# Performance work log

Hardware: AMD Instinct MI355X
Metric: run time of the kernel (lower is better)

Reference implementation:

```python
import jax, jax.numpy as jnp
import numpy as np

ALPHA = 0.3          # triplet margin
LOSS_WEIGHT = 1.0
VALID_COST = 100.0   # chosen so all queries are valid (query2gt ~ U[0,1))
POS_T = 3            # pos_thresh
NEG_T = 30           # neg_thresh
EPS = 1e-6           # torch pairwise_distance eps


def setup_inputs() -> dict:
    key0 = jax.random.key(0)
    ks = jax.random.split(key0, 6)
    Nq, V, K, D, G = 2048, 6, 4096, 256, 64
    attn = jax.random.normal(ks[0], (Nq, V, K), dtype=jnp.float32)
    query2gt = jax.random.uniform(ks[1], (Nq, G), dtype=jnp.float32)  # min < VALID_COST always
    query = jax.random.normal(ks[2], (Nq, V, D), dtype=jnp.float32)
    key = jax.random.normal(ks[3], (K, V, D), dtype=jnp.float32)
    pos_idx = jax.random.randint(ks[4], (V * Nq,), 0, POS_T, dtype=jnp.int64 if jax.config.jax_enable_x64 else jnp.int32)
    neg_idx = jax.random.randint(ks[5], (V * Nq,), POS_T, NEG_T, dtype=jnp.int64 if jax.config.jax_enable_x64 else jnp.int32)
    return {"attn": attn, "query2gt": query2gt, "query": query, "key": key,
            "pos_idx": pos_idx, "neg_idx": neg_idx}


def reference(attn, query2gt, query, key, pos_idx, neg_idx):
    # valid filtering: query2gt.min(-1) < VALID_COST is all-True by construction,
    # so no rows are dropped (keeps shapes static under jit).
    q = jnp.transpose(query, (1, 0, 2))   # [V, Nq, D]
    k = jnp.transpose(key, (1, 0, 2))     # [V, K, D]
    a = jnp.transpose(attn, (1, 0, 2))    # [V, Nq, K]
    V, Nq, K = a.shape

    # batched euclidean cdist per view via gram expansion
    qq = jnp.sum(q * q, axis=-1)[:, :, None]          # [V, Nq, 1]
    kk = jnp.sum(k * k, axis=-1)[:, None, :]          # [V, 1, K]
    d2 = qq + kk - 2.0 * jnp.einsum('vnd,vkd->vnk', q, k)
    dist = jnp.sqrt(jnp.maximum(d2, 0.0))             # [V, Nq, K]

    sorted_idx = jnp.argsort(dist, axis=-1).reshape(V * Nq, K)
    a = a.reshape(V * Nq, K)
    r = jnp.arange(V * Nq)

    pos = jax.nn.sigmoid(a[r, sorted_idx[r, pos_idx]])  # [V*Nq]
    neg = jax.nn.sigmoid(a[r, sorted_idx[r, neg_idx]])  # [V*Nq]

    # TripletMarginLoss(margin=ALPHA, p=1) with anchor = ones, 1-d embeddings
    d_pos = jnp.abs(1.0 - pos + EPS)
    d_neg = jnp.abs(1.0 - neg + EPS)
    loss = jnp.mean(jnp.maximum(d_pos - d_neg + ALPHA, 0.0))
    return LOSS_WEIGHT * loss
```

## Files before the change

### kernel.cpp

```cpp
#include <hip/hip_runtime.h>
#include <stdint.h>

#define NQ    2048
#define VV    6
#define KCNT  4096
#define DD    256
#define NROWS (VV*NQ)
#define ALPHA_M 0.3f
#define EPSL  1e-6f
#define SBIAS 256.0f
#define ZTHR  2.05f
#define CAP   256
#define LCAP  16

#define TM 128
#define TN 128
#define BKK 32

typedef _Float16 f16x8 __attribute__((ext_vector_type(8)));
typedef _Float16 f16x4 __attribute__((ext_vector_type(4)));
typedef float    f32x4 __attribute__((ext_vector_type(4)));

__device__ __forceinline__ void gload16(const void* g, void* l) {
    __builtin_amdgcn_global_load_lds(
        (__attribute__((address_space(1))) void*)(uintptr_t)g,
        (__attribute__((address_space(3))) void*)(uintptr_t)(uint32_t)(uintptr_t)l,
        16, 0, 0);
}

__device__ __forceinline__ unsigned ord16(_Float16 h) {
    unsigned short b = __builtin_bit_cast(unsigned short, h);
    return (b & 0x8000u) ? (unsigned)(~b & 0xFFFFu) : (unsigned)(b | 0x8000u);
}

__device__ __forceinline__ float triplet_term(const float* attn, int r, int kpos, int kneg) {
    int v = r / NQ, q = r - v * NQ;
    float apos = attn[(size_t)q * (VV*KCNT) + v*KCNT + kpos];
    float aneg = attn[(size_t)q * (VV*KCNT) + v*KCNT + kneg];
    float pv = 1.0f / (1.0f + expf(-apos));
    float nv = 1.0f / (1.0f + expf(-aneg));
    float dp = fabsf(1.0f - pv + EPSL);
    float dn = fabsf(1.0f - nv + EPSL);
    return fmaxf(dp - dn + ALPHA_M, 0.0f);
}

__global__ __launch_bounds__(256) void pack_k_kernel(const float* __restrict__ key,
                                                     _Float16* __restrict__ Bpack,
                                                     float* __restrict__ kkp)
{
    int wid  = threadIdx.x >> 6;
    int lane = threadIdx.x & 63;
    int rowid = blockIdx.x * 4 + wid;
    int k = rowid / 6;
    int v = rowid - k * 6;
    float4 x = *(const float4*)(key + (size_t)rowid * DD + lane * 4);
    f16x4 h;
    h.x = (_Float16)x.x; h.y = (_Float16)x.y;
    h.z = (_Float16)x.z; h.w = (_Float16)x.w;
    *(f16x4*)(Bpack + ((size_t)(v * KCNT + k)) * DD + lane * 4) = h;

    float s = x.x*x.x + x.y*x.y + x.z*x.z + x.w*x.w;
    #pragma unroll
    for (int off = 32; off >= 1; off >>= 1) s += __shfl_xor(s, off);
    if (lane == 0) kkp[v * KCNT + k] = s;
}

__global__ __launch_bounds__(256) void pack_q_kernel(const float* __restrict__ query,
                                                     _Float16* __restrict__ Apack,
                                                     float* __restrict__ Trow)
{
    int wid  = threadIdx.x >> 6;
    int lane = threadIdx.x & 63;
    int rowid = blockIdx.x * 4 + wid;
    int q = rowid / 6;
    int v = rowid - q * 6;
    float4 x = *(const float4*)(query + (size_t)rowid * DD + lane * 4);
    f16x4 h;
    h.x = (_Float16)x.x; h.y = (_Float16)x.y;
    h.z = (_Float16)x.z; h.w = (_Float16)x.w;
    *(f16x4*)(Apack + ((size_t)(v * NQ + q)) * DD + lane * 4) = h;

    float qq = x.x*x.x + x.y*x.y + x.z*x.z + x.w*x.w;
    #pragma unroll
    for (int off = 32; off >= 1; off >>= 1) qq += __shfl_xor(qq, off);
    if (lane == 0) {
        float sd = sqrtf(512.0f + 4.0f * qq);
        Trow[v * NQ + q] = 256.0f - ZTHR * sd;
    }
}

__global__ __launch_bounds__(256) void score_gemm(const _Float16* __restrict__ Apack,
                                                  const _Float16* __restrict__ Bpack,
                                                  const float* __restrict__ kkp,
                                                  const float* __restrict__ Trow,
                                                  unsigned* __restrict__ cnt,
                                                  unsigned* __restrict__ cand)
{
    __shared__ _Float16 As[TM * BKK];
    __shared__ _Float16 Bs[TN * BKK];
    __shared__ unsigned lcnt[TM];

    int tid  = threadIdx.x;
    int wid  = tid >> 6;
    int lane = tid & 63;
    int c0   = blockIdx.x * TN;
    int grow = blockIdx.y * TM;
    int v    = grow / NQ;
    int q0   = grow - v * NQ;

    int srow = (wid << 4) + (lane >> 2);
    int sseg = (lane & 3) ^ ((lane >> 2) & 3);
    const _Float16* Ag0 = Apack + ((size_t)(v*NQ   + q0 + srow)) * DD + sseg*8;
    const _Float16* Ag1 = Ag0 + (size_t)64 * DD;
    const _Float16* Bg0 = Bpack + ((size_t)(v*KCNT + c0 + srow)) * DD + sseg*8;
    const _Float16* Bg1 = Bg0 + (size_t)64 * DD;

    _Float16* lA0 = As + wid*512;
    _Float16* lA1 = As + 2048 + wid*512;
    _Float16* lB0 = Bs + wid*512;
    _Float16* lB1 = Bs + 2048 + wid*512;

    int fr = lane & 15;
    int kg = lane >> 4;
    int rb = (wid >> 1) * 64;
    int cb = (wid & 1) * 64;
    int ksw = (kg ^ (fr & 3)) << 3;

    f32x4 acc[4][4] = {};

    for (int kb = 0; kb < DD; kb += BKK) {
        __syncthreads();
        gload16(Ag0 + kb, lA0);
        gload16(Ag1 + kb, lA1);
        gload16(Bg0 + kb, lB0);
        gload16(Bg1 + kb, lB1);
        __syncthreads();

        f16x8 af[4], bf[4];
        #pragma unroll
        for (int m = 0; m < 4; ++m)
            af[m] = *(const f16x8*)&As[(rb + m*16 + fr)*BKK + ksw];
        #pragma unroll
        for (int n = 0; n < 4; ++n)
            bf[n] = *(const f16x8*)&Bs[(cb + n*16 + fr)*BKK + ksw];
        #pragma unroll
        for (int m = 0; m < 4; ++m)
            #pragma unroll
            for (int n = 0; n < 4; ++n)
                acc[m][n] = __builtin_amdgcn_mfma_f32_16x16x32_f16(af[m], bf[n], acc[m][n], 0, 0, 0);
    }

    int rg = lane >> 4;
    float kkv[4];
    #pragma unroll
    for (int n = 0; n < 4; ++n)
        kkv[n] = kkp[v*KCNT + c0 + cb + n*16 + fr];

    __syncthreads();
    unsigned* lbuf = (unsigned*)As;
    if (tid < TM) lcnt[tid] = 0;
    __syncthreads();

    #pragma unroll
    for (int m = 0; m < 4; ++m) {
        #pragma unroll
        for (int j = 0; j < 4; ++j) {
            int lr = rb + m*16 + rg*4 + j;
            float Tr = Trow[grow + lr];
            #pragma unroll
            for (int n = 0; n < 4; ++n) {
                float s = kkv[n] - 2.0f * acc[m][n][j];
                if (s < Tr) {
                    unsigned pos = atomicAdd(&lcnt[lr], 1u);
                    if (pos < LCAP)
                        lbuf[lr*LCAP + pos] =
                            (ord16((_Float16)(s - SBIAS)) << 12)
                            | (unsigned)(c0 + cb + n*16 + fr);
                }
            }
        }
    }
    __syncthreads();

    if (tid < TM) {
        unsigned c = lcnt[tid];
        int gr = grow + tid;
        if (c > LCAP) {
            atomicAdd(&cnt[gr], 100000u);
        } else if (c > 0) {
            unsigned base = atomicAdd(&cnt[gr], c);
            for (unsigned i = 0; i < c; ++i) {
                unsigned pos = base + i;
                if (pos < CAP) cand[(size_t)gr * CAP + pos] = lbuf[tid*LCAP + i];
            }
        }
    }
}

__global__ __launch_bounds__(256) void select2_kernel(const unsigned* __restrict__ cnt,
                                                      const unsigned* __restrict__ cand,
                                                      const float* __restrict__ attn,
                                                      const int* __restrict__ pos_idx,
                                                      const int* __restrict__ neg_idx,
                                                      unsigned* __restrict__ fcount,
                                                      int* __restrict__ flist,
                                                      float* __restrict__ out)
{
    __shared__ float bsum;
    if (threadIdx.x == 0) bsum = 0.0f;
    __syncthreads();

    int wid  = threadIdx.x >> 6;
    int lane = threadIdx.x & 63;
    int r    = blockIdx.x * 4 + wid;
    int p = pos_idx[r];
    int n = neg_idx[r];
    unsigned count = cnt[r];

    if (count < (unsigned)(n + 1) || count > CAP) {
        if (lane == 0) {
            unsigned i = atomicAdd(fcount, 1u);
            flist[i] = r;
        }
    } else {
        const unsigned* cr = cand + (size_t)r * CAP;
        unsigned v0 = (lane       < (int)count) ? cr[lane]       : 0xFFFFFFFFu;
        unsigned v1 = (lane + 64  < (int)count) ? cr[lane + 64]  : 0xFFFFFFFFu;
        unsigned v2 = (lane + 128 < (int)count) ? cr[lane + 128] : 0xFFFFFFFFu;
        unsigned v3 = (lane + 192 < (int)count) ? cr[lane + 192] : 0xFFFFFFFFu;
        int kpos = 0, kneg = 0;
        for (int t = 0; t <= n; ++t) {
            unsigned m01 = v0 < v1 ? v0 : v1;
            unsigned m23 = v2 < v3 ? v2 : v3;
            unsigned m = m01 < m23 ? m01 : m23;
            #pragma unroll
            for (int off = 32; off >= 1; off >>= 1) {
                unsigned o = __shfl_xor(m, off);
                m = o < m ? o : m;
            }
            if      (v0 == m) v0 = 0xFFFFFFFFu;
            else if (v1 == m) v1 = 0xFFFFFFFFu;
            else if (v2 == m) v2 = 0xFFFFFFFFu;
            else if (v3 == m) v3 = 0xFFFFFFFFu;
            if (t == p) kpos = (int)(m & 0xFFFu);
            if (t == n) kneg = (int)(m & 0xFFFu);
        }
        if (lane == 0)
            atomicAdd(&bsum, triplet_term(attn, r, kpos, kneg) * (1.0f / (float)NROWS));
    }
    __syncthreads();
    if (threadIdx.x == 0) atomicAdd(out, bsum);
}

__global__ __launch_bounds__(256) void fallback_kernel(const _Float16* __restrict__ Apack,
                                                       const _Float16* __restrict__ Bpack,
                                                       const float* __restrict__ kkp,
                                                       const float* __restrict__ attn,
                                                       const int* __restrict__ pos_idx,
                                                       const int* __restrict__ neg_idx,
                                                       const unsigned* __restrict__ fcount,
                                                       const int* __restrict__ flist,
                                                       float* __restrict__ out)
{
    __shared__ float qrow[DD];
    __shared__ unsigned keys[KCNT];
    int nf = (int)*fcount;
    for (int it = blockIdx.x; it < nf; it += gridDim.x) {
        int r = flist[it];
        int v = r / NQ, q = r - v * NQ;
        qrow[threadIdx.x] = (float)Apack[((size_t)(v*NQ + q)) * DD + threadIdx.x];
        __syncthreads();
        for (int i = 0; i < 16; ++i) {
            int c = i * 256 + threadIdx.x;
            float dot = 0.0f;
            const f16x8* bp = (const f16x8*)(Bpack + ((size_t)(v*KCNT + c)) * DD);
            for (int d8 = 0; d8 < 32; ++d8) {
                f16x8 b = bp[d8];
                #pragma unroll
                for (int j = 0; j < 8; ++j) dot += qrow[d8*8 + j] * (float)b[j];
            }
            float s = kkp[v*KCNT + c] - 2.0f * dot;
            keys[c] = (ord16((_Float16)(s - SBIAS)) << 12) | (unsigned)c;
        }
        __syncthreads();
        if (threadIdx.x < 64) {
            int lane = threadIdx.x;
            int p = pos_idx[r], n = neg_idx[r];
            unsigned prev = 0;
            int kpos = 0, kneg = 0;
            for (int t = 0; t <= n; ++t) {
                unsigned m = 0xFFFFFFFFu;
                for (int i = 0; i < 64; ++i) {
                    unsigned kk2 = keys[i*64 + lane];
                    if (kk2 > prev && kk2 < m) m = kk2;
                }
                #pragma unroll
                for (int off = 32; off >= 1; off >>= 1) {
                    unsigned o = __shfl_xor(m, off);
                    m = o < m ? o : m;
                }
                if (t == p) kpos = (int)(m & 0xFFFu);
                if (t == n) kneg = (int)(m & 0xFFFu);
                prev = m;
            }
            if (lane == 0)
                atomicAdd(out, triplet_term(attn, r, kpos, kneg) * (1.0f / (float)NROWS));
        }
        __syncthreads();
    }
}

extern "C" void kernel_launch(void* const* d_in, const int* in_sizes, int n_in,
                              void* d_out, int out_size, void* d_ws, size_t ws_size,
                              hipStream_t stream)
{
    const float* attn    = (const float*)d_in[0];
    const float* query   = (const float*)d_in[2];
    const float* key     = (const float*)d_in[3];
    const int*   pos_idx = (const int*)d_in[4];
    const int*   neg_idx = (const int*)d_in[5];
    float* out = (float*)d_out;

    char* w = (char*)d_ws;
    unsigned* cnt      = (unsigned*)(w);
    unsigned* fcount   = (unsigned*)(w + 49152);
    float*    Trow     = (float*)   (w + 49408);
    float*    kkp      = (float*)   (w + 98560);
    _Float16* Apack    = (_Float16*)(w + 196864);
    _Float16* Bpack    = (_Float16*)(w + 6488320);
    unsigned* cand     = (unsigned*)(w + 19071232);
    int*      flist    = (int*)     (w + 31654144);

    hipMemsetAsync(d_out, 0, sizeof(float), stream);
    hipMemsetAsync(d_ws, 0, 49408, stream);

    pack_k_kernel<<<6144, 256, 0, stream>>>(key, Bpack, kkp);
    pack_q_kernel<<<3072, 256, 0, stream>>>(query, Apack, Trow);

    dim3 gg(KCNT / TN, NROWS / TM);
    score_gemm<<<gg, 256, 0, stream>>>(Apack, Bpack, kkp, Trow, cnt, cand);

    select2_kernel<<<NROWS / 4, 256, 0, stream>>>(cnt, cand, attn, pos_idx, neg_idx,
                                                  fcount, flist, out);
    fallback_kernel<<<64, 256, 0, stream>>>(Apack, Bpack, kkp, attn, pos_idx, neg_idx,
                                            fcount, flist, out);
}
```

Measured before the change: 136.4 us.

## Fuse pack kernels and memsets, double-buffer GEMM loads, ballot-based candidate compaction

Merges key/query packing and workspace zeroing into a single launch, removing two memsets and one kernel launch. The score GEMM now double-buffers LDS tiles so the next K-slice loads while MFMAs run, with one barrier per step. Candidate emission replaces shared-memory per-row counters with wave ballots and prefix popcounts plus one global atomic per row group, writing directly to the candidate buffer. This removes the LCAP overflow sentinel and adds many more global atomics, which may contend.

New measurement: 149.8 us. +9.8%, slower.

```diff
diff --git a/kernel.cpp b/kernel.cpp
--- a/kernel.cpp
+++ b/kernel.cpp
@@ -11,7 +11,6 @@
 #define SBIAS 256.0f
 #define ZTHR  2.05f
 #define CAP   256
-#define LCAP  16
 
 #define TM 128
 #define TN 128
@@ -44,48 +43,53 @@
     return fmaxf(dp - dn + ALPHA_M, 0.0f);
 }
 
-__global__ __launch_bounds__(256) void pack_k_kernel(const float* __restrict__ key,
-                                                     _Float16* __restrict__ Bpack,
-                                                     float* __restrict__ kkp)
+__global__ __launch_bounds__(256) void pack_fused(const float* __restrict__ key,
+                                                  const float* __restrict__ query,
+                                                  _Float16* __restrict__ Bpack,
+                                                  _Float16* __restrict__ Apack,
+                                                  float* __restrict__ kkp,
+                                                  float* __restrict__ Trow,
+                                                  unsigned* __restrict__ cnt,
+                                                  unsigned* __restrict__ fcount,
+                                                  float* __restrict__ out)
 {
     int wid  = threadIdx.x >> 6;
     int lane = threadIdx.x & 63;
-    int rowid = blockIdx.x * 4 + wid;
-    int k = rowid / 6;
-    int v = rowid - k * 6;
-    float4 x = *(const float4*)(key + (size_t)rowid * DD + lane * 4);
-    f16x4 h;
-    h.x = (_Float16)x.x; h.y = (_Float16)x.y;
-    h.z = (_Float16)x.z; h.w = (_Float16)x.w;
-    *(f16x4*)(Bpack + ((size_t)(v * KCNT + k)) * DD + lane * 4) = h;
-
-    float s = x.x*x.x + x.y*x.y + x.z*x.z + x.w*x.w;
-    #pragma unroll
-    for (int off = 32; off >= 1; off >>= 1) s += __shfl_xor(s, off);
-    if (lane == 0) kkp[v * KCNT + k] = s;
-}
-
-__global__ __launch_bounds__(256) void pack_q_kernel(const float* __restrict__ query,
-                                                     _Float16* __restrict__ Apack,
-                                                     float* __restrict__ Trow)
-{
-    int wid  = threadIdx.x >> 6;
-    int lane = threadIdx.x & 63;
-    int rowid = blockIdx.x * 4 + wid;
-    int q = rowid / 6;
-    int v = rowid - q * 6;
-    float4 x = *(const float4*)(query + (size_t)rowid * DD + lane * 4);
-    f16x4 h;
-    h.x = (_Float16)x.x; h.y = (_Float16)x.y;
-    h.z = (_Float16)x.z; h.w = (_Float16)x.w;
-    *(f16x4*)(Apack + ((size_t)(v * NQ + q)) * DD + lane * 4) = h;
-
-    float qq = x.x*x.x + x.y*x.y + x.z*x.z + x.w*x.w;
-    #pragma unroll
-    for (int off = 32; off >= 1; off >>= 1) qq += __shfl_xor(qq, off);
-    if (lane == 0) {
-        float sd = sqrtf(512.0f + 4.0f * qq);
-        Trow[v * NQ + q] = 256.0f - ZTHR * sd;
+    if (blockIdx.x < 6144) {
+        int rowid = blockIdx.x * 4 + wid;
+        int k = rowid / 6;
+        int v = rowid - k * 6;
+        float4 x = *(const float4*)(key + (size_t)rowid * DD + lane * 4);
+        f16x4 h;
+        h.x = (_Float16)x.x; h.y = (_Float16)x.y;
+        h.z = (_Float16)x.z; h.w = (_Float16)x.w;
+        *(f16x4*)(Bpack + ((size_t)(v * KCNT + k)) * DD + lane * 4) = h;
+
+        float s = x.x*x.x + x.y*x.y + x.z*x.z + x.w*x.w;
+        #pragma unroll
+        for (int off = 32; off >= 1; off >>= 1) s += __shfl_xor(s, off);
+        if (lane == 0) kkp[v * KCNT + k] = s;
+    } else {
+        int bid2 = blockIdx.x - 6144;
+        int z = bid2 * 256 + threadIdx.x;
+        if (z < NROWS) cnt[z] = 0;
+        if (z == NROWS)     *fcount = 0;
+        if (z == NROWS + 1) out[0] = 0.0f;
+
+        int rowid = bid2 * 4 + wid;
+        int q = rowid / 6;
+        int v = rowid - q * 6;
+        float4 x = *(const float4*)(query + (size_t)rowid * DD + lane * 4);
+        f16x4 h;
+        h.x = (_Float16)x.x; h.y = (_Float16)x.y;
+        h.z = (_Float16)x.z; h.w = (_Float16)x.w;
+        *(f16x4*)(Apack + ((size_t)(v * NQ + q)) * DD + lane * 4) = h;
+
+        float qq = x.x*x.x + x.y*x.y + x.z*x.z + x.w*x.w;
+        #pragma unroll
+        for (int off = 32; off >= 1; off >>= 1) qq += __shfl_xor(qq, off);
+        if (lane == 0)
+            Trow[v * NQ + q] = 256.0f - ZTHR * sqrtf(512.0f + 4.0f * qq);
     }
 }
 
@@ -96,9 +100,8 @@
                                                   unsigned* __restrict__ cnt,
                                                   unsigned* __restrict__ cand)
 {
-    __shared__ _Float16 As[TM * BKK];
-    __shared__ _Float16 Bs[TN * BKK];
-    __shared__ unsigned lcnt[TM];
+    __shared__ _Float16 As[2][TM * BKK];
+    __shared__ _Float16 Bs[2][TN * BKK];
 
     int tid  = threadIdx.x;
     int wid  = tid >> 6;
@@ -115,83 +118,102 @@
     const _Float16* Bg0 = Bpack + ((size_t)(v*KCNT + c0 + srow)) * DD + sseg*8;
     const _Float16* Bg1 = Bg0 + (size_t)64 * DD;
 
-    _Float16* lA0 = As + wid*512;
-    _Float16* lA1 = As + 2048 + wid*512;
-    _Float16* lB0 = Bs + wid*512;
-    _Float16* lB1 = Bs + 2048 + wid*512;
-
     int fr = lane & 15;
     int kg = lane >> 4;
     int rb = (wid >> 1) * 64;
     int cb = (wid & 1) * 64;
+    int rg = lane >> 4;
     int ksw = (kg ^ (fr & 3)) << 3;
 
     f32x4 acc[4][4] = {};
 
-    for (int kb = 0; kb < DD; kb += BKK) {
-        __syncthreads();
-        gload16(Ag0 + kb, lA0);
-        gload16(Ag1 + kb, lA1);
-        gload16(Bg0 + kb, lB0);
-        gload16(Bg1 + kb, lB1);
-        __syncthreads();
-
+    gload16(Ag0, &As[0][wid*512]);
+    gload16(Ag1, &As[0][2048 + wid*512]);
+    gload16(Bg0, &Bs[0][wid*512]);
+    gload16(Bg1, &Bs[0][2048 + wid*512]);
+    __syncthreads();
+
+    #pragma unroll
+    for (int t = 0; t < 8; ++t) {
+        int cur = t & 1;
+        if (t < 7) {
+            int kb = (t + 1) * BKK;
+            gload16(Ag0 + kb, &As[cur^1][wid*512]);
+            gload16(Ag1 + kb, &As[cur^1][2048 + wid*512]);
+            gload16(Bg0 + kb, &Bs[cur^1][wid*512]);
+            gload16(Bg1 + kb, &Bs[cur^1][2048 + wid*512]);
+        }
         f16x8 af[4], bf[4];
         #pragma unroll
         for (int m = 0; m < 4; ++m)
-            af[m] = *(const f16x8*)&As[(rb + m*16 + fr)*BKK + ksw];
+            af[m] = *(const f16x8*)&As[cur][(rb + m*16 + fr)*BKK + ksw];
         #pragma unroll
         for (int n = 0; n < 4; ++n)
-            bf[n] = *(const f16x8*)&Bs[(cb + n*16 + fr)*BKK + ksw];
+            bf[n] = *(const f16x8*)&Bs[cur][(cb + n*16 + fr)*BKK + ksw];
         #pragma unroll
         for (int m = 0; m < 4; ++m)
             #pragma unroll
             for (int n = 0; n < 4; ++n)
                 acc[m][n] = __builtin_amdgcn_mfma_f32_16x16x32_f16(af[m], bf[n], acc[m][n], 0, 0, 0);
-    }
-
-    int rg = lane >> 4;
+        __syncthreads();
+    }
+
     float kkv[4];
     #pragma unroll
     for (int n = 0; n < 4; ++n)
         kkv[n] = kkp[v*KCNT + c0 + cb + n*16 + fr];
 
-    __syncthreads();
-    unsigned* lbuf = (unsigned*)As;
-    if (tid < TM) lcnt[tid] = 0;
-    __syncthreads();
-
+    float Tr[16];
+    #pragma unroll
+    for (int m = 0; m < 4; ++m)
+        #pragma unroll
+        for (int j = 0; j < 4; ++j)
+            Tr[m*4+j] = Trow[grow + rb + m*16 + rg*4 + j];
+
+    unsigned ltm = (1u << fr) - 1u;
+    int sh = rg * 16;
+
+    unsigned basev[16];
     #pragma unroll
     for (int m = 0; m < 4; ++m) {
         #pragma unroll
         for (int j = 0; j < 4; ++j) {
-            int lr = rb + m*16 + rg*4 + j;
-            float Tr = Trow[grow + lr];
+            int idx = m*4 + j;
+            unsigned long long b0 = __ballot(kkv[0] - 2.0f*acc[m][0][j] < Tr[idx]);
+            unsigned long long b1 = __ballot(kkv[1] - 2.0f*acc[m][1][j] < Tr[idx]);
+            unsigned long long b2 = __ballot(kkv[2] - 2.0f*acc[m][2][j] < Tr[idx]);
+            unsigned long long b3 = __ballot(kkv[3] - 2.0f*acc[m][3][j] < Tr[idx]);
+            unsigned rc = __popc((unsigned)(b0 >> sh) & 0xFFFFu)
+                        + __popc((unsigned)(b1 >> sh) & 0xFFFFu)
+                        + __popc((unsigned)(b2 >> sh) & 0xFFFFu)
+                        + __popc((unsigned)(b3 >> sh) & 0xFFFFu);
+            if (fr == 0)
+                basev[idx] = atomicAdd(&cnt[grow + rb + m*16 + rg*4 + j], rc);
+        }
+    }
+
+    #pragma unroll
+    for (int m = 0; m < 4; ++m) {
+        #pragma unroll
+        for (int j = 0; j < 4; ++j) {
+            int idx = m*4 + j;
+            unsigned base = __shfl(basev[idx], rg * 16);
+            int gr = grow + rb + m*16 + rg*4 + j;
+            unsigned rank = 0;
             #pragma unroll
             for (int n = 0; n < 4; ++n) {
-                float s = kkv[n] - 2.0f * acc[m][n][j];
-                if (s < Tr) {
-                    unsigned pos = atomicAdd(&lcnt[lr], 1u);
-                    if (pos < LCAP)
-                        lbuf[lr*LCAP + pos] =
+                float s = kkv[n] - 2.0f*acc[m][n][j];
+                bool tk = s < Tr[idx];
+                unsigned long long bal = __ballot(tk);
+                unsigned g16 = (unsigned)(bal >> sh) & 0xFFFFu;
+                if (tk) {
+                    unsigned pos = base + rank + __popc(g16 & ltm);
+                    if (pos < CAP)
+                        cand[(size_t)gr * CAP + pos] =
                             (ord16((_Float16)(s - SBIAS)) << 12)
                             | (unsigned)(c0 + cb + n*16 + fr);
                 }
-            }
-        }
-    }
-    __syncthreads();
-
-    if (tid < TM) {
-        unsigned c = lcnt[tid];
-        int gr = grow + tid;
-        if (c > LCAP) {
-            atomicAdd(&cnt[gr], 100000u);
-        } else if (c > 0) {
-            unsigned base = atomicAdd(&cnt[gr], c);
-            for (unsigned i = 0; i < c; ++i) {
-                unsigned pos = base + i;
-                if (pos < CAP) cand[(size_t)gr * CAP + pos] = lbuf[tid*LCAP + i];
+                rank += __popc(g16);
             }
         }
     }
@@ -331,11 +353,8 @@
     unsigned* cand     = (unsigned*)(w + 19071232);
     int*      flist    = (int*)     (w + 31654144);
 
-    hipMemsetAsync(d_out, 0, sizeof(float), stream);
-    hipMemsetAsync(d_ws, 0, 49408, stream);
-
-    pack_k_kernel<<<6144, 256, 0, stream>>>(key, Bpack, kkp);
-    pack_q_kernel<<<3072, 256, 0, stream>>>(query, Apack, Trow);
+    pack_fused<<<9216, 256, 0, stream>>>(key, query, Bpack, Apack, kkp, Trow,
+                                         cnt, fcount, out);
 
     dim3 gg(KCNT / TN, NROWS / TM);
     score_gemm<<<gg, 256, 0, stream>>>(Apack, Bpack, kkp, Trow, cnt, cand);
```

## Replace atomic candidate compaction with per-chunk ballot slots and fuse pack kernels

Applied to the files above, without the earlier changes.

The GEMM epilogue drops the shared-memory atomics, the block barriers and the global atomicAdd per row. Each wave now uses a ballot and popcount to write candidates into fixed per-chunk slots, with a per-chunk count array. The select kernel prefix-sums the 64 chunk counts and gathers candidates into LDS before the selection step. The two pack kernels are merged into one launch, which also zeroes the counters and output, so both memsets go away. The cost is a larger candidate buffer and more global traffic in select, and rows that overflow a chunk's 16 slots now go to the fallback path.

After: 129.4 us. 1.05x faster.

```diff
diff --git a/kernel.cpp b/kernel.cpp
--- a/kernel.cpp
+++ b/kernel.cpp
@@ -11,7 +11,8 @@
 #define SBIAS 256.0f
 #define ZTHR  2.05f
 #define CAP   256
-#define LCAP  16
+#define NCHUNK 64
+#define SLOTS  16
 
 #define TM 128
 #define TN 128
@@ -44,48 +45,51 @@
     return fmaxf(dp - dn + ALPHA_M, 0.0f);
 }
 
-__global__ __launch_bounds__(256) void pack_k_kernel(const float* __restrict__ key,
-                                                     _Float16* __restrict__ Bpack,
-                                                     float* __restrict__ kkp)
+__global__ __launch_bounds__(256) void pack_fused(const float* __restrict__ key,
+                                                  const float* __restrict__ query,
+                                                  _Float16* __restrict__ Bpack,
+                                                  _Float16* __restrict__ Apack,
+                                                  float* __restrict__ kkp,
+                                                  float* __restrict__ Trow,
+                                                  unsigned* __restrict__ fcount,
+                                                  float* __restrict__ out)
 {
     int wid  = threadIdx.x >> 6;
     int lane = threadIdx.x & 63;
-    int rowid = blockIdx.x * 4 + wid;
-    int k = rowid / 6;
-    int v = rowid - k * 6;
-    float4 x = *(const float4*)(key + (size_t)rowid * DD + lane * 4);
-    f16x4 h;
-    h.x = (_Float16)x.x; h.y = (_Float16)x.y;
-    h.z = (_Float16)x.z; h.w = (_Float16)x.w;
-    *(f16x4*)(Bpack + ((size_t)(v * KCNT + k)) * DD + lane * 4) = h;
-
-    float s = x.x*x.x + x.y*x.y + x.z*x.z + x.w*x.w;
-    #pragma unroll
-    for (int off = 32; off >= 1; off >>= 1) s += __shfl_xor(s, off);
-    if (lane == 0) kkp[v * KCNT + k] = s;
-}
-
-__global__ __launch_bounds__(256) void pack_q_kernel(const float* __restrict__ query,
-                                                     _Float16* __restrict__ Apack,
-                                                     float* __restrict__ Trow)
-{
-    int wid  = threadIdx.x >> 6;
-    int lane = threadIdx.x & 63;
-    int rowid = blockIdx.x * 4 + wid;
-    int q = rowid / 6;
-    int v = rowid - q * 6;
-    float4 x = *(const float4*)(query + (size_t)rowid * DD + lane * 4);
-    f16x4 h;
-    h.x = (_Float16)x.x; h.y = (_Float16)x.y;
-    h.z = (_Float16)x.z; h.w = (_Float16)x.w;
-    *(f16x4*)(Apack + ((size_t)(v * NQ + q)) * DD + lane * 4) = h;
-
-    float qq = x.x*x.x + x.y*x.y + x.z*x.z + x.w*x.w;
-    #pragma unroll
-    for (int off = 32; off >= 1; off >>= 1) qq += __shfl_xor(qq, off);
-    if (lane == 0) {
-        float sd = sqrtf(512.0f + 4.0f * qq);
-        Trow[v * NQ + q] = 256.0f - ZTHR * sd;
+    if (blockIdx.x < 6144) {
+        int rowid = blockIdx.x * 4 + wid;
+        int k = rowid / 6;
+        int v = rowid - k * 6;
+        float4 x = *(const float4*)(key + (size_t)rowid * DD + lane * 4);
+        f16x4 h;
+        h.x = (_Float16)x.x; h.y = (_Float16)x.y;
+        h.z = (_Float16)x.z; h.w = (_Float16)x.w;
+        *(f16x4*)(Bpack + ((size_t)(v * KCNT + k)) * DD + lane * 4) = h;
+
+        float s = x.x*x.x + x.y*x.y + x.z*x.z + x.w*x.w;
+        #pragma unroll
+        for (int off = 32; off >= 1; off >>= 1) s += __shfl_xor(s, off);
+        if (lane == 0) kkp[v * KCNT + k] = s;
+    } else {
+        int bid2 = blockIdx.x - 6144;
+        if (bid2 == 0) {
+            if (threadIdx.x == 0) *fcount = 0;
+            if (threadIdx.x == 1) out[0] = 0.0f;
+        }
+        int rowid = bid2 * 4 + wid;
+        int q = rowid / 6;
+        int v = rowid - q * 6;
+        float4 x = *(const float4*)(query + (size_t)rowid * DD + lane * 4);
+        f16x4 h;
+        h.x = (_Float16)x.x; h.y = (_Float16)x.y;
+        h.z = (_Float16)x.z; h.w = (_Float16)x.w;
+        *(f16x4*)(Apack + ((size_t)(v * NQ + q)) * DD + lane * 4) = h;
+
+        float qq = x.x*x.x + x.y*x.y + x.z*x.z + x.w*x.w;
+        #pragma unroll
+        for (int off = 32; off >= 1; off >>= 1) qq += __shfl_xor(qq, off);
+        if (lane == 0)
+            Trow[v * NQ + q] = 256.0f - ZTHR * sqrtf(512.0f + 4.0f * qq);
     }
 }
 
@@ -93,12 +97,11 @@
                                                   const _Float16* __restrict__ Bpack,
                                                   const float* __restrict__ kkp,
                                                   const float* __restrict__ Trow,
-                                                  unsigned* __restrict__ cnt,
+                                                  unsigned* __restrict__ cnt2,
                                                   unsigned* __restrict__ cand)
 {
     __shared__ _Float16 As[TM * BKK];
     __shared__ _Float16 Bs[TN * BKK];
-    __shared__ unsigned lcnt[TM];
 
     int tid  = threadIdx.x;
     int wid  = tid >> 6;
@@ -124,6 +127,7 @@
     int kg = lane >> 4;
     int rb = (wid >> 1) * 64;
     int cb = (wid & 1) * 64;
+    int rg = lane >> 4;
     int ksw = (kg ^ (fr & 3)) << 3;
 
     f32x4 acc[4][4] = {};
@@ -150,54 +154,47 @@
                 acc[m][n] = __builtin_amdgcn_mfma_f32_16x16x32_f16(af[m], bf[n], acc[m][n], 0, 0, 0);
     }
 
-    int rg = lane >> 4;
+    int chunk = blockIdx.x * 2 + (wid & 1);
     float kkv[4];
     #pragma unroll
     for (int n = 0; n < 4; ++n)
         kkv[n] = kkp[v*KCNT + c0 + cb + n*16 + fr];
 
-    __syncthreads();
-    unsigned* lbuf = (unsigned*)As;
-    if (tid < TM) lcnt[tid] = 0;
-    __syncthreads();
+    unsigned ltm = (1u << fr) - 1u;
+    int sh = rg * 16;
 
     #pragma unroll
     for (int m = 0; m < 4; ++m) {
         #pragma unroll
         for (int j = 0; j < 4; ++j) {
-            int lr = rb + m*16 + rg*4 + j;
-            float Tr = Trow[grow + lr];
+            int gr = grow + rb + m*16 + rg*4 + j;
+            float Tr = Trow[gr];
+            float s[4];
+            unsigned g16[4];
             #pragma unroll
             for (int n = 0; n < 4; ++n) {
-                float s = kkv[n] - 2.0f * acc[m][n][j];
-                if (s < Tr) {
-                    unsigned pos = atomicAdd(&lcnt[lr], 1u);
-                    if (pos < LCAP)
-                        lbuf[lr*LCAP + pos] =
-                            (ord16((_Float16)(s - SBIAS)) << 12)
+                s[n] = kkv[n] - 2.0f * acc[m][n][j];
+                unsigned long long bal = __ballot(s[n] < Tr);
+                g16[n] = (unsigned)(bal >> sh) & 0xFFFFu;
+            }
+            unsigned rank = 0;
+            #pragma unroll
+            for (int n = 0; n < 4; ++n) {
+                if (s[n] < Tr) {
+                    unsigned pos = rank + __popc(g16[n] & ltm);
+                    if (pos < SLOTS)
+                        cand[((size_t)gr << 10) + (chunk << 4) + pos] =
+                            (ord16((_Float16)(s[n] - SBIAS)) << 12)
                             | (unsigned)(c0 + cb + n*16 + fr);
                 }
-            }
-        }
-    }
-    __syncthreads();
-
-    if (tid < TM) {
-        unsigned c = lcnt[tid];
-        int gr = grow + tid;
-        if (c > LCAP) {
-            atomicAdd(&cnt[gr], 100000u);
-        } else if (c > 0) {
-            unsigned base = atomicAdd(&cnt[gr], c);
-            for (unsigned i = 0; i < c; ++i) {
-                unsigned pos = base + i;
-                if (pos < CAP) cand[(size_t)gr * CAP + pos] = lbuf[tid*LCAP + i];
-            }
-        }
-    }
-}
-
-__global__ __launch_bounds__(256) void select2_kernel(const unsigned* __restrict__ cnt,
+                rank += __popc(g16[n]);
+            }
+            if (fr == 0) cnt2[(gr << 6) + chunk] = rank;
+        }
+    }
+}
+
+__global__ __launch_bounds__(256) void select2_kernel(const unsigned* __restrict__ cnt2,
                                                       const unsigned* __restrict__ cand,
                                                       const float* __restrict__ attn,
                                                       const int* __restrict__ pos_idx,
@@ -206,6 +203,7 @@
                                                       int* __restrict__ flist,
                                                       float* __restrict__ out)
 {
+    __shared__ unsigned cbuf[4][CAP];
     __shared__ float bsum;
     if (threadIdx.x == 0) bsum = 0.0f;
     __syncthreads();
@@ -215,19 +213,33 @@
     int r    = blockIdx.x * 4 + wid;
     int p = pos_idx[r];
     int n = neg_idx[r];
-    unsigned count = cnt[r];
-
-    if (count < (unsigned)(n + 1) || count > CAP) {
+
+    unsigned c_l = cnt2[(r << 6) + lane];
+    unsigned pre = c_l;
+    #pragma unroll
+    for (int off = 1; off <= 32; off <<= 1) {
+        unsigned o = __shfl_up(pre, off);
+        if (lane >= off) pre += o;
+    }
+    unsigned total = __shfl(pre, 63);
+    unsigned excl  = pre - c_l;
+    bool overflow  = __any(c_l > SLOTS);
+
+    if (overflow || total < (unsigned)(n + 1) || total > CAP) {
         if (lane == 0) {
             unsigned i = atomicAdd(fcount, 1u);
             flist[i] = r;
         }
     } else {
-        const unsigned* cr = cand + (size_t)r * CAP;
-        unsigned v0 = (lane       < (int)count) ? cr[lane]       : 0xFFFFFFFFu;
-        unsigned v1 = (lane + 64  < (int)count) ? cr[lane + 64]  : 0xFFFFFFFFu;
-        unsigned v2 = (lane + 128 < (int)count) ? cr[lane + 128] : 0xFFFFFFFFu;
-        unsigned v3 = (lane + 192 < (int)count) ? cr[lane + 192] : 0xFFFFFFFFu;
+        unsigned* mybuf = cbuf[wid];
+        const unsigned* src = cand + ((size_t)r << 10) + (lane << 4);
+        for (unsigned i = 0; i < c_l; ++i) mybuf[excl + i] = src[i];
+        __asm__ volatile("s_waitcnt lgkmcnt(0)" ::: "memory");
+
+        unsigned v0 = (lane       < (int)total) ? mybuf[lane]       : 0xFFFFFFFFu;
+        unsigned v1 = (lane + 64  < (int)total) ? mybuf[lane + 64]  : 0xFFFFFFFFu;
+        unsigned v2 = (lane + 128 < (int)total) ? mybuf[lane + 128] : 0xFFFFFFFFu;
+        unsigned v3 = (lane + 192 < (int)total) ? mybuf[lane + 192] : 0xFFFFFFFFu;
         int kpos = 0, kneg = 0;
         for (int t = 0; t <= n; ++t) {
             unsigned m01 = v0 < v1 ? v0 : v1;
@@ -322,25 +334,22 @@
     float* out = (float*)d_out;
 
     char* w = (char*)d_ws;
-    unsigned* cnt      = (unsigned*)(w);
-    unsigned* fcount   = (unsigned*)(w + 49152);
-    float*    Trow     = (float*)   (w + 49408);
-    float*    kkp      = (float*)   (w + 98560);
-    _Float16* Apack    = (_Float16*)(w + 196864);
-    _Float16* Bpack    = (_Float16*)(w + 6488320);
-    unsigned* cand     = (unsigned*)(w + 19071232);
-    int*      flist    = (int*)     (w + 31654144);
-
-    hipMemsetAsync(d_out, 0, sizeof(float), stream);
-    hipMemsetAsync(d_ws, 0, 49408, stream);
-
-    pack_k_kernel<<<6144, 256, 0, stream>>>(key, Bpack, kkp);
-    pack_q_kernel<<<3072, 256, 0, stream>>>(query, Apack, Trow);
+    unsigned* fcount   = (unsigned*)(w);
+    float*    Trow     = (float*)   (w + 256);
+    float*    kkp      = (float*)   (w + 49408);
+    unsigned* cnt2     = (unsigned*)(w + 147712);
+    int*      flist    = (int*)     (w + 3293440);
+    _Float16* Apack    = (_Float16*)(w + 3342592);
+    _Float16* Bpack    = (_Float16*)(w + 9634048);
+    unsigned* cand     = (unsigned*)(w + 22216960);
+
+    pack_fused<<<9216, 256, 0, stream>>>(key, query, Bpack, Apack, kkp, Trow,
+                                         fcount, out);
 
     dim3 gg(KCNT / TN, NROWS / TM);
-    score_gemm<<<gg, 256, 0, stream>>>(Apack, Bpack, kkp, Trow, cnt, cand);
-
-    select2_kernel<<<NROWS / 4, 256, 0, stream>>>(cnt, cand, attn, pos_idx, neg_idx,
+    score_gemm<<<gg, 256, 0, stream>>>(Apack, Bpack, kkp, Trow, cnt2, cand);
+
+    select2_kernel<<<NROWS / 4, 256, 0, stream>>>(cnt2, cand, attn, pos_idx, neg_idx,
                                                   fcount, flist, out);
     fallback_kernel<<<64, 256, 0, stream>>>(Apack, Bpack, kkp, attn, pos_idx, neg_idx,
                                             fcount, flist, out);
```
